# Optimization experiments

Hardware: AMD Instinct MI355X
Metric: run time of the kernel (lower is better)

The kernel has to match this reference:

```python
import jax, jax.numpy as jnp
import numpy as np

B, N, T, CIN, COUT, K, DIL = 8, 207, 12, 64, 64, 3, 1


def setup_inputs() -> dict:
    key = jax.random.key(0)
    ks = jax.random.split(key, 13)
    s = 0.05
    return {
        "X": jax.random.normal(ks[0], (B, N, T, CIN), jnp.float32),
        "wA": jax.random.normal(ks[1], (COUT, CIN, 1, K), jnp.float32) * s,
        "bA": jax.random.normal(ks[2], (COUT,), jnp.float32) * s,
        "wB": jax.random.normal(ks[3], (COUT, CIN, 1, K), jnp.float32) * s,
        "bB": jax.random.normal(ks[4], (COUT,), jnp.float32) * s,
        "wq": jax.random.normal(ks[5], (COUT // 8, COUT), jnp.float32) * s,
        "bq": jax.random.normal(ks[6], (COUT // 8,), jnp.float32) * s,
        "wk": jax.random.normal(ks[7], (COUT // 8, COUT), jnp.float32) * s,
        "bk": jax.random.normal(ks[8], (COUT // 8,), jnp.float32) * s,
        "wv": jax.random.normal(ks[9], (COUT, COUT), jnp.float32) * s,
        "bv": jax.random.normal(ks[10], (COUT,), jnp.float32) * s,
        "gamma": jax.random.normal(ks[11], (1,), jnp.float32) * 0.1,
    }


def reference(X, wA, bA, wB, bB, wq, bq, wk, bk, wv, bv, gamma):
    # X: [B, N, T, C] -> [B, C, N, T]
    x = jnp.transpose(X, (0, 3, 1, 2))
    k_size = wA.shape[-1]
    pad = (k_size - 1) * DIL  # causal left pad == pad-both + drop-right in torch code

    def causal_conv(w, b):
        y = jax.lax.conv_general_dilated(
            x, w, window_strides=(1, 1),
            padding=((0, 0), (pad, 0)),
            rhs_dilation=(1, DIL),
            dimension_numbers=("NCHW", "OIHW", "NCHW"))
        return y + b[None, :, None, None]

    A = causal_conv(wA, bA)
    Bg = causal_conv(wB, bB)
    h = A * jax.nn.sigmoid(Bg)  # [B, C, N, T]

    b_, c, w_, h_ = h.shape
    L = w_ * h_
    h2 = h.reshape(b_, c, L)  # [B, C, L]
    q = jnp.einsum("oc,bcl->bol", wq, h2) + bq[None, :, None]  # [B, C/8, L]
    kk = jnp.einsum("oc,bcl->bol", wk, h2) + bk[None, :, None]
    v = jnp.einsum("oc,bcl->bol", wv, h2) + bv[None, :, None]   # [B, C, L]

    energy = jnp.einsum("bql,bqm->blm", q, kk)  # [B, L, L]
    attn = jax.nn.softmax(energy, axis=-1)
    out = jnp.einsum("bcm,blm->bcl", v, attn).reshape(b_, c, w_, h_)
    out = gamma[0] * out + h
    return jnp.transpose(out, (0, 2, 3, 1))  # [B, N, T, C]
```

## Files before the change

### kernel.cpp

```cpp
#include <hip/hip_runtime.h>
#include <hip/hip_bf16.h>

#define Bn 8
#define Nn 207
#define Tn 12
#define Cn 64
#define Ln (Nn*Tn)
#define LP 2496
#define NT 39
#define NRB 156

typedef unsigned int u32;
typedef unsigned short u16;
typedef _Float16 f16;
typedef __fp16 h16;
typedef __attribute__((ext_vector_type(2))) __fp16 h16x2;
typedef __attribute__((ext_vector_type(4))) __fp16 h16x4;
typedef __attribute__((ext_vector_type(4))) float floatx4;

#define LOG2E 1.44269504088896f

__device__ __forceinline__ u16 f2h(float f) { f16 h = (f16)f; return *(u16*)&h; }
__device__ __forceinline__ float h2f_lo(u32 u) { u16 x = (u16)u;        f16 h = *(f16*)&x; return (float)h; }
__device__ __forceinline__ float h2f_hi(u32 u) { u16 x = (u16)(u >> 16); f16 h = *(f16*)&x; return (float)h; }

#define W_PW   0
#define U_WVT  24576
#define F_WK   14336
#define F_WQ   14848
#define U_K    30720
#define U_Q    190464
#define U_HT   350208

__global__ __launch_bounds__(256) void prep_kernel(
    const float* __restrict__ wA, const float* __restrict__ wB,
    const float* __restrict__ wq, const float* __restrict__ wk,
    const float* __restrict__ wv, float* __restrict__ ws)
{
    u16* wsu = (u16*)ws;
    u32* wsw = (u32*)ws;
    int idx = blockIdx.x * 256 + threadIdx.x;
    if (idx < 12288) {
        int co = idx & 63, j = (idx >> 6) & 7, cig = (idx >> 9) & 7, k = idx >> 12;
        int src = (co*64 + cig*8 + j)*3 + k;
        wsw[W_PW + idx] = (u32)f2h(wA[src]) | ((u32)f2h(wB[src]) << 16);
    } else if (idx < 16384) {
        int j = idx - 12288;
        wsu[U_WVT + j] = f2h(wv[j]);
    } else if (idx < 16896) {
        int j = idx - 16384; int o = j & 7, c = j >> 3;
        ws[F_WK + j] = wk[o*Cn + c];
    } else if (idx < 17408) {
        int j = idx - 16896; int o = j & 7, c = j >> 3;
        ws[F_WQ + j] = wq[o*Cn + c] * LOG2E;
    } else if (idx < 18944) {
        int j = idx - 17408;
        int b = j / 192, rem = j - b*192;
        int which = rem / 96, rr = rem - which*96;
        wsu[(which ? U_Q : U_K) + (size_t)b*LP*8 + Ln*8 + rr] = 0;
    } else if (idx < 25088) {
        int j = idx - 18944;
        int b = j / 768, rem = j - b*768;
        int c = rem / 12, mm = 52 + (rem - c*12);
        int ss = mm >> 4, q = (mm >> 2) & 3, i = mm & 3;
        int cs = c >> 4, rm = c & 15;
        int fidx = ss*4 + cs;
        wsu[U_HT + (size_t)b*NT*4096 + 38*4096
            + (fidx >> 1)*512 + (rm*4 + q)*8 + (fidx & 1)*4 + i] = 0;
    }
}

__global__ __launch_bounds__(256, 2) void conv_k_kernel(
    const float* __restrict__ X,
    const float* __restrict__ bA, const float* __restrict__ bB,
    const float* __restrict__ bk, const float* __restrict__ bq,
    float* __restrict__ ws, float* __restrict__ out)
{
    __shared__ u32   w_s[6144];
    __shared__ float xs[Tn*Cn];
    __shared__ float hs[Tn*Cn];
    __shared__ float wkq_s[1024];
    int b = blockIdx.x & 7;
    int n = blockIdx.x >> 3;
    int tid = threadIdx.x;

    const u32* wsw = (const u32*)ws;
    #pragma unroll
    for (int i = 0; i < 6; ++i) {
        int d4 = i*256 + tid;
        int co4 = d4 & 15, j = (d4 >> 4) & 7, cl = (d4 >> 7) & 3, k = d4 >> 9;
        ((uint4*)w_s)[d4] = ((const uint4*)(wsw + W_PW))[((k*8 + cl)*8 + j)*16 + co4];
    }
    const float* Xp = X + (size_t)(b*Nn + n)*Tn*Cn;
    if (tid < 192)
        ((float4*)xs)[tid] = ((const float4*)Xp)[tid];
    ((float4*)wkq_s)[tid] = ((const float4*)(ws + F_WK))[tid];
    __syncthreads();

    int co = tid & 63;
    int tg = tid >> 6;
    float aA[3] = {bA[co], bA[co], bA[co]};
    float aB[3] = {bB[co], bB[co], bB[co]};
    int tb = tg*3 - 2;

    #pragma unroll 1
    for (int half = 0; half < 2; ++half) {
        #pragma unroll 1
        for (int cl = 0; cl < 4; ++cl) {
            int cig = half*4 + cl;
            float xr[5][8];
            #pragma unroll
            for (int d = 0; d < 5; ++d) {
                int tp = tb + d;
                if (tp >= 0) {
                    float4 xa = *(const float4*)(xs + tp*Cn + cig*8);
                    float4 xb = *(const float4*)(xs + tp*Cn + cig*8 + 4);
                    xr[d][0]=xa.x; xr[d][1]=xa.y; xr[d][2]=xa.z; xr[d][3]=xa.w;
                    xr[d][4]=xb.x; xr[d][5]=xb.y; xr[d][6]=xb.z; xr[d][7]=xb.w;
                } else {
                    #pragma unroll
                    for (int j = 0; j < 8; ++j) xr[d][j] = 0.f;
                }
            }
            #pragma unroll
            for (int k = 0; k < 3; ++k) {
                #pragma unroll
                for (int j = 0; j < 8; ++j) {
                    u32 p = w_s[((k*4 + cl)*8 + j)*64 + co];
                    float wa = h2f_lo(p), wb = h2f_hi(p);
                    #pragma unroll
                    for (int tt = 0; tt < 3; ++tt) {
                        aA[tt] += xr[tt + k][j] * wa;
                        aB[tt] += xr[tt + k][j] * wb;
                    }
                }
            }
        }
        if (half == 0) {
            __syncthreads();
            #pragma unroll
            for (int i = 0; i < 6; ++i) {
                int d4 = i*256 + tid;
                int co4 = d4 & 15, j = (d4 >> 4) & 7, cl = (d4 >> 7) & 3, k = d4 >> 9;
                ((uint4*)w_s)[d4] =
                    ((const uint4*)(wsw + W_PW))[((k*8 + 4 + cl)*8 + j)*16 + co4];
            }
            __syncthreads();
        }
    }

    #pragma unroll
    for (int tt = 0; tt < 3; ++tt) {
        int t = tg*3 + tt;
        float hv = aA[tt] * (1.f / (1.f + __expf(-aB[tt])));
        hs[t*Cn + co] = hv;
        out[((size_t)b*Ln + (size_t)n*Tn + t)*Cn + co] = hv;
    }
    __syncthreads();

    if (tid < 96) {
        int r = tid >> 3, o = tid & 7;
        float acc = bk[o];
        for (int ci = 0; ci < Cn; ++ci) {
            int c = (ci + r) & 63;
            acc += hs[r*Cn + c] * wkq_s[c*8 + o];
        }
        ((u16*)ws)[U_K + (size_t)b*LP*8 + ((size_t)n*Tn + r)*8 + o] = f2h(acc);
    } else if (tid < 192) {
        int r = (tid - 96) >> 3, o = tid & 7;
        float acc = bq[o] * LOG2E;
        for (int ci = 0; ci < Cn; ++ci) {
            int c = (ci + r) & 63;
            acc += hs[r*Cn + c] * wkq_s[512 + c*8 + o];
        }
        ((u16*)ws)[U_Q + (size_t)b*LP*8 + ((size_t)n*Tn + r)*8 + o] = f2h(acc);
    }
    {
        int jj = tid >> 6, c = tid & 63;
        if (jj < 3) {
            int m = n*Tn + 4*jj;
            int tile = m >> 6, mloc = m & 63;
            int ss = mloc >> 4, q = (mloc >> 2) & 3;
            int cs = c >> 4, rm = c & 15;
            u32 p0 = ((u32)f2h(hs[(4*jj+1)*Cn + c]) << 16) | f2h(hs[(4*jj+0)*Cn + c]);
            u32 p1 = ((u32)f2h(hs[(4*jj+3)*Cn + c]) << 16) | f2h(hs[(4*jj+2)*Cn + c]);
            int fidx = ss*4 + cs;
            u16* ht = (u16*)ws + U_HT + (size_t)b*NT*4096 + tile*4096
                    + (fidx >> 1)*512 + (rm*4 + q)*8 + (fidx & 1)*4;
            *(uint2*)ht = make_uint2(p0, p1);
        }
    }
}

__global__ __launch_bounds__(256, 3) void attn_kernel(
    const float* __restrict__ gamma, const float* __restrict__ bv,
    const float* __restrict__ ws, float* __restrict__ out)
{
    __shared__ float part[4*64*16];
    __shared__ float den_part[4][16];

    int b  = blockIdx.x & 7;
    int rb = blockIdx.x >> 3;
    int R0 = rb*16;
    int tid = threadIdx.x;
    int lane = tid & 63;
    int w = tid >> 6;
    int rm = lane & 15;
    int quad = lane >> 4;

    const u16* wsu = (const u16*)ws;
    const u16* kb = wsu + U_K  + (size_t)b*LP*8;
    const u16* qb = wsu + U_Q  + (size_t)b*LP*8;
    const u16* hb = wsu + U_HT + (size_t)b*NT*4096;

    h16x4 qf0;
    {
        uint2 u0 = make_uint2(0, 0);
        int r0 = R0 + rm;
        if (quad < 2)
            u0 = *(const uint2*)(qb + (size_t)r0*8 + 4*quad);
        qf0 = *(h16x4*)&u0;
    }

    const h16x2 one2 = {(h16)1.f, (h16)1.f};

    floatx4 acc[4];
    #pragma unroll
    for (int cs = 0; cs < 4; ++cs) acc[cs] = (floatx4){0.f, 0.f, 0.f, 0.f};
    float dsum0 = 0.f;

    uint2 k0_0,k0_1,k0_2,k0_3, k1_0,k1_1,k1_2,k1_3;
    uint4 hp_0,hp_1,hp_2,hp_3,hp_4,hp_5,hp_6,hp_7;

#define LDK(kt, SS) ((quad < 2) ? *(const uint2*)((kt) + ((SS)*16 + rm)*8 + 4*quad) : make_uint2(0,0))
#define LDH4(ht, P) (*(const uint4*)((ht) + (P)*512 + lane*8))

#define LOADK(B, T) {                                                          \
    int tc = ((T) < NT) ? (T) : (NT-1);                                        \
    const u16* kt_ = kb + (size_t)tc*512;                                      \
    k##B##_0 = LDK(kt_, 0); k##B##_1 = LDK(kt_, 1);                            \
    k##B##_2 = LDK(kt_, 2); k##B##_3 = LDK(kt_, 3);                            \
}

#define LOADH(T) {                                                             \
    int tc = ((T) < NT) ? (T) : (NT-1);                                        \
    const u16* ht_ = hb + (size_t)tc*4096;                                     \
    hp_0 = LDH4(ht_, 0); hp_1 = LDH4(ht_, 1);                                  \
    hp_2 = LDH4(ht_, 2); hp_3 = LDH4(ht_, 3);                                  \
    hp_4 = LDH4(ht_, 4); hp_5 = LDH4(ht_, 5);                                  \
    hp_6 = LDH4(ht_, 6); hp_7 = LDH4(ht_, 7);                                  \
}

#define COMPSS(KR, PA, PB) {                                                   \
    h16x4 kf = *(h16x4*)&KR;                                                   \
    floatx4 s0 = {0.f,0.f,0.f,0.f};                                            \
    s0 = __builtin_amdgcn_mfma_f32_16x16x16f16(kf, qf0, s0, 0, 0, 0);          \
    h16x2 e0a = __builtin_amdgcn_cvt_pkrtz(__builtin_amdgcn_exp2f(s0[0]),      \
                                           __builtin_amdgcn_exp2f(s0[1]));     \
    h16x2 e0b = __builtin_amdgcn_cvt_pkrtz(__builtin_amdgcn_exp2f(s0[2]),      \
                                           __builtin_amdgcn_exp2f(s0[3]));     \
    dsum0 = __builtin_amdgcn_fdot2(e0a, one2, dsum0, false);                   \
    dsum0 = __builtin_amdgcn_fdot2(e0b, one2, dsum0, false);                   \
    h16x4 e0 = __builtin_shufflevector(e0a, e0b, 0, 1, 2, 3);                  \
    h16x4 a0_ = *(h16x4*)&PA.x, a1_ = *(h16x4*)&PA.z;                          \
    h16x4 a2_ = *(h16x4*)&PB.x, a3_ = *(h16x4*)&PB.z;                          \
    acc[0] = __builtin_amdgcn_mfma_f32_16x16x16f16(a0_, e0, acc[0], 0, 0, 0);  \
    acc[1] = __builtin_amdgcn_mfma_f32_16x16x16f16(a1_, e0, acc[1], 0, 0, 0);  \
    acc[2] = __builtin_amdgcn_mfma_f32_16x16x16f16(a2_, e0, acc[2], 0, 0, 0);  \
    acc[3] = __builtin_amdgcn_mfma_f32_16x16x16f16(a3_, e0, acc[3], 0, 0, 0);  \
}

#define COMPT(B) {                                                             \
    __builtin_amdgcn_s_setprio(1);                                             \
    COMPSS(k##B##_0, hp_0, hp_1)                                               \
    COMPSS(k##B##_1, hp_2, hp_3)                                               \
    COMPSS(k##B##_2, hp_4, hp_5)                                               \
    COMPSS(k##B##_3, hp_6, hp_7)                                               \
    __builtin_amdgcn_s_setprio(0);                                             \
}

    LOADK(0, w)
    LOADH(w)
    for (int i = 0; i < 4; ++i) {
        int t0 = w + 8*i;
        LOADK(1, t0 + 4)
        COMPT(0)
        LOADH(t0 + 4)
        LOADK(0, t0 + 8)
        COMPT(1)
        LOADH(t0 + 8)
    }
    LOADK(1, w + 36)
    COMPT(0)
    if (w < 3) {
        LOADH(w + 36)
        COMPT(1)
    }
#undef LOADK
#undef LOADH
#undef COMPT
#undef COMPSS
#undef LDK
#undef LDH4

    {
        float s_ = dsum0;
        s_ += __shfl_xor(s_, 16, 64);
        s_ += __shfl_xor(s_, 32, 64);
        if (quad == 0) den_part[w][rm] = s_;
    }

    float* pw = part + w*1024;
    #pragma unroll
    for (int cs = 0; cs < 4; ++cs)
        #pragma unroll
        for (int i = 0; i < 4; ++i)
            pw[(cs*16 + quad*4 + i)*16 + rm] = acc[cs][i];
    __syncthreads();

    for (int j = tid; j < 1024; j += 256)
        part[j] = part[j] + part[1024 + j] + part[2048 + j] + part[3072 + j];
    __syncthreads();

    int o = tid & 63, rq = tid >> 6;
    float gam = gamma[0];
    float bvo = bv[o];
    const u16* wvr = wsu + U_WVT + o*64;
    uint4 wvu[8];
    #pragma unroll
    for (int x = 0; x < 8; ++x) wvu[x] = *(const uint4*)(wvr + x*8);
    #pragma unroll
    for (int rr = 0; rr < 4; ++rr) {
        int r = rq*4 + rr;
        int row = R0 + r;
        if (row < Ln) {
            float den = den_part[0][r] + den_part[1][r] + den_part[2][r] + den_part[3][r]
                      - 12.0f;
            float p = 0.f;
            #pragma unroll
            for (int x = 0; x < 8; ++x) {
                const f16* hh = (const f16*)&wvu[x];
                #pragma unroll
                for (int i = 0; i < 8; ++i)
                    p += (float)hh[i] * part[(x*8 + i)*16 + r];
            }
            size_t gi = ((size_t)b*Ln + row)*64 + o;
            out[gi] = gam*(bvo + p/den) + out[gi];
        }
    }
}

extern "C" void kernel_launch(void* const* d_in, const int* in_sizes, int n_in,
                              void* d_out, int out_size, void* d_ws, size_t ws_size,
                              hipStream_t stream) {
    const float* X     = (const float*)d_in[0];
    const float* wA    = (const float*)d_in[1];
    const float* bA    = (const float*)d_in[2];
    const float* wB    = (const float*)d_in[3];
    const float* bB    = (const float*)d_in[4];
    const float* wq    = (const float*)d_in[5];
    const float* bq    = (const float*)d_in[6];
    const float* wk    = (const float*)d_in[7];
    const float* bk    = (const float*)d_in[8];
    const float* wv    = (const float*)d_in[9];
    const float* bv    = (const float*)d_in[10];
    const float* gamma = (const float*)d_in[11];
    float* out = (float*)d_out;
    float* ws  = (float*)d_ws;

    prep_kernel<<<98, 256, 0, stream>>>(wA, wB, wq, wk, wv, ws);
    conv_k_kernel<<<Bn*Nn, 256, 0, stream>>>(X, bA, bB, bk, bq, ws, out);
    attn_kernel<<<Bn*NRB, 256, 0, stream>>>(gamma, bv, ws, out);
}
```

Before: 142.3 us.

## Process two graph nodes per conv block to amortize weight staging

Each conv block now handles two nodes (n0 and n0+104) instead of one. It loads both X slices and reuses the same staged fp16 conv weights in shared memory for both. This halves the number of blocks and the repeated weight loads into LDS. In exchange, each block holds more registers and runs longer, the second node's epilogue is serialized with extra barriers, and the grid shrinks from 1656 to 832 blocks.

Result: slower. 154.5 us (+8.6%).

```diff
diff --git a/kernel.cpp b/kernel.cpp
--- a/kernel.cpp
+++ b/kernel.cpp
@@ -9,6 +9,7 @@
 #define LP 2496
 #define NT 39
 #define NRB 156
+#define NBC 104
 
 typedef unsigned int u32;
 typedef unsigned short u16;
@@ -77,117 +78,147 @@
     float* __restrict__ ws, float* __restrict__ out)
 {
     __shared__ u32   w_s[6144];
-    __shared__ float xs[Tn*Cn];
+    __shared__ float xs[2][Tn*Cn];
     __shared__ float hs[Tn*Cn];
     __shared__ float wkq_s[1024];
-    int b = blockIdx.x & 7;
-    int n = blockIdx.x >> 3;
     int tid = threadIdx.x;
+    int b  = blockIdx.x & 7;
+    int n0 = blockIdx.x >> 3;
+    int n1 = n0 + NBC;
+    bool two = (n1 < Nn);
+
+    ((float4*)wkq_s)[tid] = ((const float4*)(ws + F_WK))[tid];
 
     const u32* wsw = (const u32*)ws;
-    #pragma unroll
-    for (int i = 0; i < 6; ++i) {
-        int d4 = i*256 + tid;
-        int co4 = d4 & 15, j = (d4 >> 4) & 7, cl = (d4 >> 7) & 3, k = d4 >> 9;
-        ((uint4*)w_s)[d4] = ((const uint4*)(wsw + W_PW))[((k*8 + cl)*8 + j)*16 + co4];
-    }
-    const float* Xp = X + (size_t)(b*Nn + n)*Tn*Cn;
-    if (tid < 192)
-        ((float4*)xs)[tid] = ((const float4*)Xp)[tid];
-    ((float4*)wkq_s)[tid] = ((const float4*)(ws + F_WK))[tid];
+#define STAGEW(HALF) {                                                         \
+    _Pragma("unroll")                                                          \
+    for (int i = 0; i < 6; ++i) {                                              \
+        int d4 = i*256 + tid;                       \
+        int co4 = d4 & 15, j = (d4 >> 4) & 7, cl = (d4 >> 7) & 3, k = d4 >> 9; \
+        ((uint4*)w_s)[d4] =                                                    \
+            ((const uint4*)(wsw + W_PW))[((k*8 + (HALF)*4 + cl)*8 + j)*16 + co4]; \
+    }                                                                          \
+}
+    STAGEW(0)
+    {
+        const float* Xp0 = X + (size_t)(b*Nn + n0)*Tn*Cn;
+        const float* Xp1 = X + (size_t)(b*Nn + n1)*Tn*Cn;
+        if (tid < 192) ((float4*)xs[0])[tid] = ((const float4*)Xp0)[tid];
+        else if (two)  ((float4*)xs[1])[tid - 192] = ((const float4*)Xp1)[tid - 192];
+        if (two && tid < 128)
+            ((float4*)xs[1])[64 + tid] = ((const float4*)Xp1)[64 + tid];
+    }
     __syncthreads();
 
     int co = tid & 63;
     int tg = tid >> 6;
-    float aA[3] = {bA[co], bA[co], bA[co]};
-    float aB[3] = {bB[co], bB[co], bB[co]};
     int tb = tg*3 - 2;
+    float bAv = bA[co], bBv = bB[co];
+    int o_ = tid & 7;
+    float bko = 0.f;
+    if (tid < 96) bko = bk[o_];
+    else if (tid < 192) bko = bq[o_] * LOG2E;
+
+    float aA[2][3], aB[2][3];
+    #pragma unroll
+    for (int ni = 0; ni < 2; ++ni)
+        #pragma unroll
+        for (int tt = 0; tt < 3; ++tt) { aA[ni][tt] = 0.f; aB[ni][tt] = 0.f; }
 
     #pragma unroll 1
     for (int half = 0; half < 2; ++half) {
         #pragma unroll 1
         for (int cl = 0; cl < 4; ++cl) {
             int cig = half*4 + cl;
-            float xr[5][8];
             #pragma unroll
-            for (int d = 0; d < 5; ++d) {
-                int tp = tb + d;
-                if (tp >= 0) {
-                    float4 xa = *(const float4*)(xs + tp*Cn + cig*8);
-                    float4 xb = *(const float4*)(xs + tp*Cn + cig*8 + 4);
-                    xr[d][0]=xa.x; xr[d][1]=xa.y; xr[d][2]=xa.z; xr[d][3]=xa.w;
-                    xr[d][4]=xb.x; xr[d][5]=xb.y; xr[d][6]=xb.z; xr[d][7]=xb.w;
-                } else {
+            for (int ni = 0; ni < 2; ++ni) {
+                if (ni == 0 || two) {
+                    const float* xsp = xs[ni];
+                    float xr[5][8];
                     #pragma unroll
-                    for (int j = 0; j < 8; ++j) xr[d][j] = 0.f;
-                }
-            }
-            #pragma unroll
-            for (int k = 0; k < 3; ++k) {
-                #pragma unroll
-                for (int j = 0; j < 8; ++j) {
-                    u32 p = w_s[((k*4 + cl)*8 + j)*64 + co];
-                    float wa = h2f_lo(p), wb = h2f_hi(p);
+                    for (int d = 0; d < 5; ++d) {
+                        int tp = tb + d;
+                        if (tp >= 0) {
+                            float4 xa = *(const float4*)(xsp + tp*Cn + cig*8);
+                            float4 xb = *(const float4*)(xsp + tp*Cn + cig*8 + 4);
+                            xr[d][0]=xa.x; xr[d][1]=xa.y; xr[d][2]=xa.z; xr[d][3]=xa.w;
+                            xr[d][4]=xb.x; xr[d][5]=xb.y; xr[d][6]=xb.z; xr[d][7]=xb.w;
+                        } else {
+                            #pragma unroll
+                            for (int j = 0; j < 8; ++j) xr[d][j] = 0.f;
+                        }
+                    }
                     #pragma unroll
-                    for (int tt = 0; tt < 3; ++tt) {
-                        aA[tt] += xr[tt + k][j] * wa;
-                        aB[tt] += xr[tt + k][j] * wb;
+                    for (int k = 0; k < 3; ++k) {
+                        #pragma unroll
+                        for (int j = 0; j < 8; ++j) {
+                            u32 p = w_s[((k*4 + cl)*8 + j)*64 + co];
+                            float wa = h2f_lo(p), wb = h2f_hi(p);
+                            #pragma unroll
+                            for (int tt = 0; tt < 3; ++tt) {
+                                aA[ni][tt] += xr[tt + k][j] * wa;
+                                aB[ni][tt] += xr[tt + k][j] * wb;
+                            }
+                        }
                     }
                 }
             }
         }
         if (half == 0) {
             __syncthreads();
+            STAGEW(1)
+            __syncthreads();
+        }
+    }
+#undef STAGEW
+
+    u16* wsu16 = (u16*)ws;
+    #pragma unroll
+    for (int ni = 0; ni < 2; ++ni) {
+        if (ni == 0 || two) {
+            int n = ni ? n1 : n0;
+            __syncthreads();
             #pragma unroll
-            for (int i = 0; i < 6; ++i) {
-                int d4 = i*256 + tid;
-                int co4 = d4 & 15, j = (d4 >> 4) & 7, cl = (d4 >> 7) & 3, k = d4 >> 9;
-                ((uint4*)w_s)[d4] =
-                    ((const uint4*)(wsw + W_PW))[((k*8 + 4 + cl)*8 + j)*16 + co4];
+            for (int tt = 0; tt < 3; ++tt) {
+                int t = tg*3 + tt;
+                float sA = aA[ni][tt] + bAv, sB = aB[ni][tt] + bBv;
+                float hv = sA * (1.f / (1.f + __expf(-sB)));
+                hs[t*Cn + co] = hv;
+                out[((size_t)b*Ln + (size_t)n*Tn + t)*Cn + co] = hv;
             }
             __syncthreads();
-        }
-    }
-
-    #pragma unroll
-    for (int tt = 0; tt < 3; ++tt) {
-        int t = tg*3 + tt;
-        float hv = aA[tt] * (1.f / (1.f + __expf(-aB[tt])));
-        hs[t*Cn + co] = hv;
-        out[((size_t)b*Ln + (size_t)n*Tn + t)*Cn + co] = hv;
-    }
-    __syncthreads();
-
-    if (tid < 96) {
-        int r = tid >> 3, o = tid & 7;
-        float acc = bk[o];
-        for (int ci = 0; ci < Cn; ++ci) {
-            int c = (ci + r) & 63;
-            acc += hs[r*Cn + c] * wkq_s[c*8 + o];
-        }
-        ((u16*)ws)[U_K + (size_t)b*LP*8 + ((size_t)n*Tn + r)*8 + o] = f2h(acc);
-    } else if (tid < 192) {
-        int r = (tid - 96) >> 3, o = tid & 7;
-        float acc = bq[o] * LOG2E;
-        for (int ci = 0; ci < Cn; ++ci) {
-            int c = (ci + r) & 63;
-            acc += hs[r*Cn + c] * wkq_s[512 + c*8 + o];
-        }
-        ((u16*)ws)[U_Q + (size_t)b*LP*8 + ((size_t)n*Tn + r)*8 + o] = f2h(acc);
-    }
-    {
-        int jj = tid >> 6, c = tid & 63;
-        if (jj < 3) {
-            int m = n*Tn + 4*jj;
-            int tile = m >> 6, mloc = m & 63;
-            int ss = mloc >> 4, q = (mloc >> 2) & 3;
-            int cs = c >> 4, rm = c & 15;
-            u32 p0 = ((u32)f2h(hs[(4*jj+1)*Cn + c]) << 16) | f2h(hs[(4*jj+0)*Cn + c]);
-            u32 p1 = ((u32)f2h(hs[(4*jj+3)*Cn + c]) << 16) | f2h(hs[(4*jj+2)*Cn + c]);
-            int fidx = ss*4 + cs;
-            u16* ht = (u16*)ws + U_HT + (size_t)b*NT*4096 + tile*4096
-                    + (fidx >> 1)*512 + (rm*4 + q)*8 + (fidx & 1)*4;
-            *(uint2*)ht = make_uint2(p0, p1);
+            if (tid < 96) {
+                int r = tid >> 3;
+                float acc = bko;
+                for (int ci = 0; ci < Cn; ++ci) {
+                    int c = (ci + r) & 63;
+                    acc += hs[r*Cn + c] * wkq_s[c*8 + o_];
+                }
+                wsu16[U_K + (size_t)b*LP*8 + ((size_t)n*Tn + r)*8 + o_] = f2h(acc);
+            } else if (tid < 192) {
+                int r = (tid - 96) >> 3;
+                float acc = bko;
+                for (int ci = 0; ci < Cn; ++ci) {
+                    int c = (ci + r) & 63;
+                    acc += hs[r*Cn + c] * wkq_s[512 + c*8 + o_];
+                }
+                wsu16[U_Q + (size_t)b*LP*8 + ((size_t)n*Tn + r)*8 + o_] = f2h(acc);
+            }
+            {
+                int jj = tid >> 6, c = tid & 63;
+                if (jj < 3) {
+                    int m = n*Tn + 4*jj;
+                    int tile = m >> 6, mloc = m & 63;
+                    int ss = mloc >> 4, q = (mloc >> 2) & 3;
+                    int cs = c >> 4, rm = c & 15;
+                    u32 p0 = ((u32)f2h(hs[(4*jj+1)*Cn + c]) << 16) | f2h(hs[(4*jj+0)*Cn + c]);
+                    u32 p1 = ((u32)f2h(hs[(4*jj+3)*Cn + c]) << 16) | f2h(hs[(4*jj+2)*Cn + c]);
+                    int fidx = ss*4 + cs;
+                    u16* ht = wsu16 + U_HT + (size_t)b*NT*4096 + tile*4096
+                            + (fidx >> 1)*512 + (rm*4 + q)*8 + (fidx & 1)*4;
+                    *(uint2*)ht = make_uint2(p0, p1);
+                }
+            }
         }
     }
 }
@@ -369,6 +400,6 @@
     float* ws  = (float*)d_ws;
 
     prep_kernel<<<98, 256, 0, stream>>>(wA, wB, wq, wk, wv, ws);
-    conv_k_kernel<<<Bn*Nn, 256, 0, stream>>>(X, bA, bB, bk, bq, ws, out);
+    conv_k_kernel<<<Bn*NBC, 256, 0, stream>>>(X, bA, bB, bk, bq, ws, out);
     attn_kernel<<<Bn*NRB, 256, 0, stream>>>(gamma, bv, ws, out);
 }
```
